# Kernel optimization log

Hardware: AMD Instinct MI355X
Metric: run time of the kernel (lower is better)

The kernel has to match this reference:

```python
import math
import jax, jax.numpy as jnp
import numpy as np

N_HEADS = 16
D_MODEL = 1024
B, S = 1, 2048


def setup_inputs() -> dict:
    key = jax.random.key(0)
    ks = jax.random.split(key, 8)
    stdv = 1.0 / math.sqrt(D_MODEL)
    def w(k):
        return jax.random.uniform(k, (D_MODEL, D_MODEL), jnp.float32, -stdv, stdv)
    return {
        "query": jax.random.normal(ks[0], (B, S, D_MODEL), jnp.float32),
        "key": jax.random.normal(ks[1], (B, S, D_MODEL), jnp.float32),
        "value": jax.random.normal(ks[2], (B, S, D_MODEL), jnp.float32),
        "attn_mask": jax.random.randint(ks[3], (B, S, S), 0, 2, jnp.int32),
        "W_q": w(ks[4]),
        "W_k": w(ks[5]),
        "W_v": w(ks[6]),
        "W_o": w(ks[7]),
    }


def reference(query, key, value, attn_mask, W_q, W_k, W_v, W_o):
    b = query.shape[0]
    d = D_MODEL // N_HEADS
    # F.linear(x, W) = x @ W.T
    def proj(x, W):
        y = jnp.einsum('bse,de->bsd', x, W)  # [B,S,D]
        return y.reshape(b, -1, N_HEADS, d).transpose(0, 2, 1, 3)  # [B,H,S,d]
    q = proj(query, W_q)
    k = proj(key, W_k)
    v = proj(value, W_v)
    scores = jnp.einsum('bhsd,bhtd->bhst', q, k) / math.sqrt(d)  # [B,H,S,S]
    # masked_fill with -1e-07 where mask is truthy (faithful to source)
    mask = (attn_mask != 0)[:, None, :, :]  # broadcast over heads
    scores = jnp.where(mask, jnp.float32(-1e-07), scores)
    attn_scores = jax.nn.softmax(scores, axis=-1)
    # Faithful quirk: output uses PRE-softmax scores, not attn_scores
    out = jnp.einsum('bhst,bhtd->bhsd', scores, v)
    concat = out.transpose(0, 2, 1, 3).reshape(b, -1, D_MODEL)
    output = jnp.einsum('bse,de->bsd', concat, W_o)
    return output, attn_scores
```

## Files before the change

kernel.cpp:

```cpp
#include <hip/hip_runtime.h>

#define S 2048
#define DM 1024
#define H 16
#define DH 64

typedef __attribute__((ext_vector_type(8))) short bf16x8;
typedef __attribute__((ext_vector_type(4))) float f32x4;
typedef __attribute__((ext_vector_type(4))) unsigned short u16x4;
typedef unsigned short u16;
typedef unsigned int u32;

__device__ __forceinline__ void split2(float x, u16& h, u16& l) {
  const u32 u = __float_as_uint(x);
  const u32 hu = u & 0xFFFF0000u;
  h = (u16)(hu >> 16);
  const float rem = x - __uint_as_float(hu);
  u32 r = __float_as_uint(rem);
  r += 0x7FFFu + ((r >> 16) & 1u);
  l = (u16)(r >> 16);
}

__device__ __forceinline__ void split2v(float x, u16x4& h4, u16x4& l4, int i) {
  u16 hh, ll;
  split2(x, hh, ll);
  h4[i] = hh; l4[i] = ll;
}

__device__ __forceinline__ f32x4 mfma3(bf16x8 ah, bf16x8 al, bf16x8 bh, bf16x8 bl, f32x4 c) {
  c = __builtin_amdgcn_mfma_f32_16x16x32_bf16(ah, bh, c, 0, 0, 0);
  c = __builtin_amdgcn_mfma_f32_16x16x32_bf16(ah, bl, c, 0, 0, 0);
  c = __builtin_amdgcn_mfma_f32_16x16x32_bf16(al, bh, c, 0, 0, 0);
  return c;
}

__global__ __launch_bounds__(256)
void qkv_proj(const float* __restrict__ q, const float* __restrict__ k,
              const float* __restrict__ v, const float* __restrict__ Wq,
              const float* __restrict__ Wk, const float* __restrict__ Wv,
              u16* __restrict__ qh, u16* __restrict__ ql,
              u16* __restrict__ kh, u16* __restrict__ kl,
              u16* __restrict__ vTh, u16* __restrict__ vTl)
{
  __shared__ u16 Ah[128][40], Al[128][40], Bh[128][40], Bl[128][40];
  const int tid = threadIdx.x;
  const int lane = tid & 63, w = tid >> 6;
  const int wr = w >> 1, wc = w & 1;
  const int lg = lane >> 4, lt = lane & 15;
  const int z = blockIdx.z;

  const float *A, *B;
  int m0, n0;
  if (z == 2) { A = Wv; B = v; m0 = blockIdx.y * 128; n0 = blockIdx.x * 128; }
  else {
    A = (z == 0) ? q : k; B = (z == 0) ? Wq : Wk;
    m0 = blockIdx.x * 128; n0 = blockIdx.y * 128;
  }

  f32x4 acc[4][4] = {};

  for (int k0 = 0; k0 < DM; k0 += 32) {
    float4 av[4], bv[4];
#pragma unroll
    for (int p = 0; p < 4; p++) {
      const int idx = p * 256 + tid;
      const int row = idx >> 3, c4 = (idx & 7) * 4;
      av[p] = *(const float4*)&A[(size_t)(m0 + row) * DM + k0 + c4];
      bv[p] = *(const float4*)&B[(size_t)(n0 + row) * DM + k0 + c4];
    }
    __syncthreads();
#pragma unroll
    for (int p = 0; p < 4; p++) {
      const int idx = p * 256 + tid;
      const int row = idx >> 3, c4 = (idx & 7) * 4;
      u16x4 h4, l4;
      split2v(av[p].x, h4, l4, 0); split2v(av[p].y, h4, l4, 1);
      split2v(av[p].z, h4, l4, 2); split2v(av[p].w, h4, l4, 3);
      *(u16x4*)&Ah[row][c4] = h4; *(u16x4*)&Al[row][c4] = l4;
      split2v(bv[p].x, h4, l4, 0); split2v(bv[p].y, h4, l4, 1);
      split2v(bv[p].z, h4, l4, 2); split2v(bv[p].w, h4, l4, 3);
      *(u16x4*)&Bh[row][c4] = h4; *(u16x4*)&Bl[row][c4] = l4;
    }
    __syncthreads();

    bf16x8 bhf[4], blf[4];
#pragma unroll
    for (int fj = 0; fj < 4; fj++) {
      const int r = wc * 64 + fj * 16 + lt;
      bhf[fj] = *(const bf16x8*)&Bh[r][lg * 8];
      blf[fj] = *(const bf16x8*)&Bl[r][lg * 8];
    }
#pragma unroll
    for (int fi = 0; fi < 4; fi++) {
      const int r = wr * 64 + fi * 16 + lt;
      const bf16x8 ahf = *(const bf16x8*)&Ah[r][lg * 8];
      const bf16x8 alf = *(const bf16x8*)&Al[r][lg * 8];
#pragma unroll
      for (int fj = 0; fj < 4; fj++)
        acc[fi][fj] = mfma3(ahf, alf, bhf[fj], blf[fj], acc[fi][fj]);
    }
  }

  u16 *dh, *dl;
  float scale;
  if (z == 0)      { dh = qh;  dl = ql;  scale = 0.125f; }
  else if (z == 1) { dh = kh;  dl = kl;  scale = 1.0f; }
  else             { dh = vTh; dl = vTl; scale = 1.0f; }

#pragma unroll
  for (int fi = 0; fi < 4; fi++)
#pragma unroll
    for (int r = 0; r < 4; r++) {
      const int m = m0 + wr * 64 + fi * 16 + lg * 4 + r;
#pragma unroll
      for (int fj = 0; fj < 4; fj++) {
        const int n = n0 + wc * 64 + fj * 16 + lt;
        const size_t addr = (z == 2) ? ((size_t)m * S + n)
                                     : ((size_t)((n >> 6) * S + m) * 64 + (n & 63));
        u16 hh, ll;
        split2(acc[fi][fj][r] * scale, hh, ll);
        dh[addr] = hh; dl[addr] = ll;
      }
    }
}

__global__ __launch_bounds__(256)
void attn_pv(const u16* __restrict__ qh, const u16* __restrict__ ql,
             const u16* __restrict__ kh, const u16* __restrict__ kl,
             const u16* __restrict__ vTh, const u16* __restrict__ vTl,
             const int* __restrict__ mask,
             float* __restrict__ attn, u16* __restrict__ ch, u16* __restrict__ cl)
{
  __shared__ u16 Kh[64][72], Kl[64][72];
  __shared__ u16 Vh[64][72], Vl[64][72];
  __shared__ u16 Ph[64][72], Pl[64][72];
  const int tid = threadIdx.x;
  const int lane = tid & 63, w = tid >> 6;
  const int lg = lane >> 4, lt = lane & 15;
  const int h = blockIdx.y, s0 = blockIdx.x * 64;
  const int qrow = s0 + w * 16 + lt;

  const size_t qbase = ((size_t)h * S + qrow) * 64;
  bf16x8 Qh_[2], Ql_[2];
  Qh_[0] = *(const bf16x8*)&qh[qbase + lg * 8];
  Qh_[1] = *(const bf16x8*)&qh[qbase + 32 + lg * 8];
  Ql_[0] = *(const bf16x8*)&ql[qbase + lg * 8];
  Ql_[1] = *(const bf16x8*)&ql[qbase + 32 + lg * 8];

  const size_t kbase = (size_t)h * S * 64;
  const size_t vbase = (size_t)h * 64 * S;

  f32x4 ao[4] = {};
  float m_run = -3.0e38f, l_run = 0.0f;

  for (int t0 = 0; t0 < S; t0 += 64) {
    __syncthreads();
#pragma unroll
    for (int p = 0; p < 2; p++) {
      const int chunk = p * 256 + tid;
      const int row = chunk >> 3, c8 = (chunk & 7) * 8;
      *(uint4*)&Kh[row][c8] = *(const uint4*)&kh[kbase + (size_t)(t0 + row) * 64 + c8];
      *(uint4*)&Kl[row][c8] = *(const uint4*)&kl[kbase + (size_t)(t0 + row) * 64 + c8];
      *(uint4*)&Vh[row][c8] = *(const uint4*)&vTh[vbase + (size_t)row * S + t0 + c8];
      *(uint4*)&Vl[row][c8] = *(const uint4*)&vTl[vbase + (size_t)row * S + t0 + c8];
    }
    __syncthreads();

    f32x4 sct[4] = {};
#pragma unroll
    for (int ks = 0; ks < 2; ks++) {
#pragma unroll
      for (int ft = 0; ft < 4; ft++) {
        const bf16x8 ah = *(const bf16x8*)&Kh[ft * 16 + lt][ks * 32 + lg * 8];
        const bf16x8 al = *(const bf16x8*)&Kl[ft * 16 + lt][ks * 32 + lg * 8];
        sct[ft] = mfma3(ah, al, Qh_[ks], Ql_[ks], sct[ft]);
      }
    }

    const int* mrow = &mask[(size_t)qrow * S + t0];
    float pm = -3.0e38f;
#pragma unroll
    for (int ft = 0; ft < 4; ft++) {
      const int tl = ft * 16 + lg * 4;
      const int4 mv = *(const int4*)&mrow[tl];
      f32x4 sv = sct[ft];
      sv[0] = mv.x ? -1e-7f : sv[0];
      sv[1] = mv.y ? -1e-7f : sv[1];
      sv[2] = mv.z ? -1e-7f : sv[2];
      sv[3] = mv.w ? -1e-7f : sv[3];
      sct[ft] = sv;
      pm = fmaxf(pm, fmaxf(fmaxf(sv[0], sv[1]), fmaxf(sv[2], sv[3])));
      u16x4 h4, l4;
      split2v(sv[0], h4, l4, 0); split2v(sv[1], h4, l4, 1);
      split2v(sv[2], h4, l4, 2); split2v(sv[3], h4, l4, 3);
      *(u16x4*)&Ph[w * 16 + lt][tl] = h4;
      *(u16x4*)&Pl[w * 16 + lt][tl] = l4;
    }

    pm = fmaxf(pm, __shfl_xor(pm, 16));
    pm = fmaxf(pm, __shfl_xor(pm, 32));
    const float mn = fmaxf(m_run, pm);
    float es = 0.0f;
#pragma unroll
    for (int ft = 0; ft < 4; ft++) {
      es += __expf(sct[ft][0] - mn) + __expf(sct[ft][1] - mn)
          + __expf(sct[ft][2] - mn) + __expf(sct[ft][3] - mn);
    }
    es += __shfl_xor(es, 16);
    es += __shfl_xor(es, 32);
    l_run = l_run * __expf(m_run - mn) + es;
    m_run = mn;

#pragma unroll
    for (int ks = 0; ks < 2; ks++) {
      const bf16x8 pa_h = *(const bf16x8*)&Ph[w * 16 + lt][ks * 32 + lg * 8];
      const bf16x8 pa_l = *(const bf16x8*)&Pl[w * 16 + lt][ks * 32 + lg * 8];
#pragma unroll
      for (int fd = 0; fd < 4; fd++) {
        const bf16x8 vb_h = *(const bf16x8*)&Vh[fd * 16 + lt][ks * 32 + lg * 8];
        const bf16x8 vb_l = *(const bf16x8*)&Vl[fd * 16 + lt][ks * 32 + lg * 8];
        ao[fd] = mfma3(pa_h, pa_l, vb_h, vb_l, ao[fd]);
      }
    }
  }

#pragma unroll
  for (int fd = 0; fd < 4; fd++)
#pragma unroll
    for (int r = 0; r < 4; r++) {
      const int qg = s0 + w * 16 + lg * 4 + r;
      const int d = h * 64 + fd * 16 + lt;
      u16 hh, ll;
      split2(ao[fd][r], hh, ll);
      ch[(size_t)qg * DM + d] = hh;
      cl[(size_t)qg * DM + d] = ll;
    }

  const float fm  = m_run;
  const float fil = 1.0f / l_run;

  for (int t0 = 0; t0 < S; t0 += 64) {
    __syncthreads();
#pragma unroll
    for (int p = 0; p < 2; p++) {
      const int chunk = p * 256 + tid;
      const int row = chunk >> 3, c8 = (chunk & 7) * 8;
      *(uint4*)&Kh[row][c8] = *(const uint4*)&kh[kbase + (size_t)(t0 + row) * 64 + c8];
      *(uint4*)&Kl[row][c8] = *(const uint4*)&kl[kbase + (size_t)(t0 + row) * 64 + c8];
    }
    __syncthreads();

    f32x4 sct[4] = {};
#pragma unroll
    for (int ks = 0; ks < 2; ks++) {
#pragma unroll
      for (int ft = 0; ft < 4; ft++) {
        const bf16x8 ah = *(const bf16x8*)&Kh[ft * 16 + lt][ks * 32 + lg * 8];
        const bf16x8 al = *(const bf16x8*)&Kl[ft * 16 + lt][ks * 32 + lg * 8];
        sct[ft] = mfma3(ah, al, Qh_[ks], Ql_[ks], sct[ft]);
      }
    }

    const int* mrow = &mask[(size_t)qrow * S + t0];
    float* arow = &attn[((size_t)h * S + qrow) * S + t0];
#pragma unroll
    for (int ft = 0; ft < 4; ft++) {
      const int tl = ft * 16 + lg * 4;
      const int4 mv = *(const int4*)&mrow[tl];
      f32x4 sv = sct[ft];
      sv[0] = mv.x ? -1e-7f : sv[0];
      sv[1] = mv.y ? -1e-7f : sv[1];
      sv[2] = mv.z ? -1e-7f : sv[2];
      sv[3] = mv.w ? -1e-7f : sv[3];
      const float4 o = make_float4(__expf(sv[0] - fm) * fil,
                                   __expf(sv[1] - fm) * fil,
                                   __expf(sv[2] - fm) * fil,
                                   __expf(sv[3] - fm) * fil);
      *(float4*)&arow[tl] = o;
    }
  }
}

__global__ __launch_bounds__(256)
void out_proj(const u16* __restrict__ ch, const u16* __restrict__ cl,
              const float* __restrict__ Wo, float* __restrict__ out)
{
  __shared__ u16 Ah[128][40], Al[128][40], Bh[128][40], Bl[128][40];
  const int tid = threadIdx.x;
  const int lane = tid & 63, w = tid >> 6;
  const int wr = w >> 1, wc = w & 1;
  const int lg = lane >> 4, lt = lane & 15;
  const int m0 = blockIdx.x * 128, n0 = blockIdx.y * 128;

  f32x4 acc[4][4] = {};

  for (int k0 = 0; k0 < DM; k0 += 32) {
    uint4 ahv[2], alv[2];
    float4 bv[4];
#pragma unroll
    for (int p = 0; p < 2; p++) {
      const int chunk = p * 256 + tid;
      const int row = chunk >> 2, c8 = (chunk & 3) * 8;
      ahv[p] = *(const uint4*)&ch[(size_t)(m0 + row) * DM + k0 + c8];
      alv[p] = *(const uint4*)&cl[(size_t)(m0 + row) * DM + k0 + c8];
    }
#pragma unroll
    for (int p = 0; p < 4; p++) {
      const int idx = p * 256 + tid;
      const int row = idx >> 3, c4 = (idx & 7) * 4;
      bv[p] = *(const float4*)&Wo[(size_t)(n0 + row) * DM + k0 + c4];
    }
    __syncthreads();
#pragma unroll
    for (int p = 0; p < 2; p++) {
      const int chunk = p * 256 + tid;
      const int row = chunk >> 2, c8 = (chunk & 3) * 8;
      *(uint4*)&Ah[row][c8] = ahv[p];
      *(uint4*)&Al[row][c8] = alv[p];
    }
#pragma unroll
    for (int p = 0; p < 4; p++) {
      const int idx = p * 256 + tid;
      const int row = idx >> 3, c4 = (idx & 7) * 4;
      u16x4 h4, l4;
      split2v(bv[p].x, h4, l4, 0); split2v(bv[p].y, h4, l4, 1);
      split2v(bv[p].z, h4, l4, 2); split2v(bv[p].w, h4, l4, 3);
      *(u16x4*)&Bh[row][c4] = h4; *(u16x4*)&Bl[row][c4] = l4;
    }
    __syncthreads();

    bf16x8 bhf[4], blf[4];
#pragma unroll
    for (int fj = 0; fj < 4; fj++) {
      const int r = wc * 64 + fj * 16 + lt;
      bhf[fj] = *(const bf16x8*)&Bh[r][lg * 8];
      blf[fj] = *(const bf16x8*)&Bl[r][lg * 8];
    }
#pragma unroll
    for (int fi = 0; fi < 4; fi++) {
      const int r = wr * 64 + fi * 16 + lt;
      const bf16x8 ahf = *(const bf16x8*)&Ah[r][lg * 8];
      const bf16x8 alf = *(const bf16x8*)&Al[r][lg * 8];
#pragma unroll
      for (int fj = 0; fj < 4; fj++)
        acc[fi][fj] = mfma3(ahf, alf, bhf[fj], blf[fj], acc[fi][fj]);
    }
  }

#pragma unroll
  for (int fi = 0; fi < 4; fi++)
#pragma unroll
    for (int r = 0; r < 4; r++) {
      const int m = m0 + wr * 64 + fi * 16 + lg * 4 + r;
#pragma unroll
      for (int fj = 0; fj < 4; fj++) {
        const int n = n0 + wc * 64 + fj * 16 + lt;
        out[(size_t)m * DM + n] = acc[fi][fj][r];
      }
    }
}

extern "C" void kernel_launch(void* const* d_in, const int* in_sizes, int n_in,
                              void* d_out, int out_size, void* d_ws, size_t ws_size,
                              hipStream_t stream)
{
  const float* query = (const float*)d_in[0];
  const float* key   = (const float*)d_in[1];
  const float* value = (const float*)d_in[2];
  const int*   mask  = (const int*)d_in[3];
  const float* Wq    = (const float*)d_in[4];
  const float* Wk    = (const float*)d_in[5];
  const float* Wv    = (const float*)d_in[6];
  const float* Wo    = (const float*)d_in[7];

  float* out  = (float*)d_out;
  float* attn = out + (size_t)S * DM;

  const size_t NE = (size_t)H * S * 64;
  u16* qh  = (u16*)d_ws;
  u16* ql  = qh  + NE;
  u16* kh  = ql  + NE;
  u16* kl  = kh  + NE;
  u16* vTh = kl  + NE;
  u16* vTl = vTh + NE;
  u16* ch  = vTl + NE;
  u16* cl  = ch  + NE;

  hipLaunchKernelGGL(qkv_proj, dim3(16, 8, 3), dim3(256), 0, stream,
                     query, key, value, Wq, Wk, Wv, qh, ql, kh, kl, vTh, vTl);

  hipLaunchKernelGGL(attn_pv, dim3(S / 64, H), dim3(256), 0, stream,
                     qh, ql, kh, kl, vTh, vTl, mask, attn, ch, cl);

  hipLaunchKernelGGL(out_proj, dim3(16, 8), dim3(256), 0, stream,
                     ch, cl, Wo, out);
}
```

Baseline: 579.6 us.

## Restructure attention kernel around 32x32 MFMA with register-resident P and split-key waves

```diff
diff --git a/kernel.cpp b/kernel.cpp
--- a/kernel.cpp
+++ b/kernel.cpp
@@ -7,7 +7,9 @@
 
 typedef __attribute__((ext_vector_type(8))) short bf16x8;
 typedef __attribute__((ext_vector_type(4))) float f32x4;
+typedef __attribute__((ext_vector_type(16))) float f32x16;
 typedef __attribute__((ext_vector_type(4))) unsigned short u16x4;
+typedef __attribute__((ext_vector_type(4))) unsigned int u32x4;
 typedef unsigned short u16;
 typedef unsigned int u32;
 
@@ -20,17 +22,32 @@
   r += 0x7FFFu + ((r >> 16) & 1u);
   l = (u16)(r >> 16);
 }
-
 __device__ __forceinline__ void split2v(float x, u16x4& h4, u16x4& l4, int i) {
   u16 hh, ll;
   split2(x, hh, ll);
   h4[i] = hh; l4[i] = ll;
 }
+__device__ __forceinline__ u32 pack_split_hi(float a, float b) {
+  return (__float_as_uint(a) >> 16) | (__float_as_uint(b) & 0xFFFF0000u);
+}
+__device__ __forceinline__ u32 pack_split_lo(float a, float b) {
+  const float ra = a - __uint_as_float(__float_as_uint(a) & 0xFFFF0000u);
+  const float rb = b - __uint_as_float(__float_as_uint(b) & 0xFFFF0000u);
+  u32 ua = __float_as_uint(ra); ua += 0x7FFFu + ((ua >> 16) & 1u);
+  u32 ub = __float_as_uint(rb); ub += 0x7FFFu + ((ub >> 16) & 1u);
+  return (ua >> 16) | (ub & 0xFFFF0000u);
+}
 
 __device__ __forceinline__ f32x4 mfma3(bf16x8 ah, bf16x8 al, bf16x8 bh, bf16x8 bl, f32x4 c) {
   c = __builtin_amdgcn_mfma_f32_16x16x32_bf16(ah, bh, c, 0, 0, 0);
   c = __builtin_amdgcn_mfma_f32_16x16x32_bf16(ah, bl, c, 0, 0, 0);
   c = __builtin_amdgcn_mfma_f32_16x16x32_bf16(al, bh, c, 0, 0, 0);
+  return c;
+}
+__device__ __forceinline__ f32x16 mfma3w(bf16x8 ah, bf16x8 al, bf16x8 bh, bf16x8 bl, f32x16 c) {
+  c = __builtin_amdgcn_mfma_f32_32x32x16_bf16(ah, bh, c, 0, 0, 0);
+  c = __builtin_amdgcn_mfma_f32_32x32x16_bf16(ah, bl, c, 0, 0, 0);
+  c = __builtin_amdgcn_mfma_f32_32x32x16_bf16(al, bh, c, 0, 0, 0);
   return c;
 }
 
@@ -124,33 +141,36 @@
     }
 }
 
-__global__ __launch_bounds__(256)
+__global__ __launch_bounds__(256, 3)
 void attn_pv(const u16* __restrict__ qh, const u16* __restrict__ ql,
              const u16* __restrict__ kh, const u16* __restrict__ kl,
              const u16* __restrict__ vTh, const u16* __restrict__ vTl,
              const int* __restrict__ mask,
              float* __restrict__ attn, u16* __restrict__ ch, u16* __restrict__ cl)
 {
-  __shared__ u16 Kh[64][72], Kl[64][72];
-  __shared__ u16 Vh[64][72], Vl[64][72];
-  __shared__ u16 Ph[64][72], Pl[64][72];
+  __shared__ u16 KV[4][64][72];
+  __shared__ float mbuf[2][64], lbuf[2][64];
+  float* sc = (float*)&KV[0][0][0];
+
   const int tid = threadIdx.x;
   const int lane = tid & 63, w = tid >> 6;
-  const int lg = lane >> 4, lt = lane & 15;
+  const int wq = w >> 1, wt = w & 1;
+  const int l31 = lane & 31, hi = lane >> 5;
   const int h = blockIdx.y, s0 = blockIdx.x * 64;
-  const int qrow = s0 + w * 16 + lt;
+  const int qrow = s0 + wq * 32 + l31;
 
   const size_t qbase = ((size_t)h * S + qrow) * 64;
-  bf16x8 Qh_[2], Ql_[2];
-  Qh_[0] = *(const bf16x8*)&qh[qbase + lg * 8];
-  Qh_[1] = *(const bf16x8*)&qh[qbase + 32 + lg * 8];
-  Ql_[0] = *(const bf16x8*)&ql[qbase + lg * 8];
-  Ql_[1] = *(const bf16x8*)&ql[qbase + 32 + lg * 8];
+  bf16x8 Qh_[4], Ql_[4];
+#pragma unroll
+  for (int ts = 0; ts < 4; ts++) {
+    Qh_[ts] = *(const bf16x8*)&qh[qbase + ts * 16 + hi * 8];
+    Ql_[ts] = *(const bf16x8*)&ql[qbase + ts * 16 + hi * 8];
+  }
 
   const size_t kbase = (size_t)h * S * 64;
   const size_t vbase = (size_t)h * 64 * S;
 
-  f32x4 ao[4] = {};
+  f32x16 ao0 = {}, ao1 = {};
   float m_run = -3.0e38f, l_run = 0.0f;
 
   for (int t0 = 0; t0 < S; t0 += 64) {
@@ -159,85 +179,117 @@
     for (int p = 0; p < 2; p++) {
       const int chunk = p * 256 + tid;
       const int row = chunk >> 3, c8 = (chunk & 7) * 8;
-      *(uint4*)&Kh[row][c8] = *(const uint4*)&kh[kbase + (size_t)(t0 + row) * 64 + c8];
-      *(uint4*)&Kl[row][c8] = *(const uint4*)&kl[kbase + (size_t)(t0 + row) * 64 + c8];
-      *(uint4*)&Vh[row][c8] = *(const uint4*)&vTh[vbase + (size_t)row * S + t0 + c8];
-      *(uint4*)&Vl[row][c8] = *(const uint4*)&vTl[vbase + (size_t)row * S + t0 + c8];
-    }
-    __syncthreads();
-
-    f32x4 sct[4] = {};
-#pragma unroll
-    for (int ks = 0; ks < 2; ks++) {
-#pragma unroll
-      for (int ft = 0; ft < 4; ft++) {
-        const bf16x8 ah = *(const bf16x8*)&Kh[ft * 16 + lt][ks * 32 + lg * 8];
-        const bf16x8 al = *(const bf16x8*)&Kl[ft * 16 + lt][ks * 32 + lg * 8];
-        sct[ft] = mfma3(ah, al, Qh_[ks], Ql_[ks], sct[ft]);
-      }
-    }
-
-    const int* mrow = &mask[(size_t)qrow * S + t0];
-    float pm = -3.0e38f;
-#pragma unroll
-    for (int ft = 0; ft < 4; ft++) {
-      const int tl = ft * 16 + lg * 4;
-      const int4 mv = *(const int4*)&mrow[tl];
-      f32x4 sv = sct[ft];
-      sv[0] = mv.x ? -1e-7f : sv[0];
-      sv[1] = mv.y ? -1e-7f : sv[1];
-      sv[2] = mv.z ? -1e-7f : sv[2];
-      sv[3] = mv.w ? -1e-7f : sv[3];
-      sct[ft] = sv;
-      pm = fmaxf(pm, fmaxf(fmaxf(sv[0], sv[1]), fmaxf(sv[2], sv[3])));
-      u16x4 h4, l4;
-      split2v(sv[0], h4, l4, 0); split2v(sv[1], h4, l4, 1);
-      split2v(sv[2], h4, l4, 2); split2v(sv[3], h4, l4, 3);
-      *(u16x4*)&Ph[w * 16 + lt][tl] = h4;
-      *(u16x4*)&Pl[w * 16 + lt][tl] = l4;
-    }
-
-    pm = fmaxf(pm, __shfl_xor(pm, 16));
+      *(uint4*)&KV[0][row][c8] = *(const uint4*)&kh[kbase + (size_t)(t0 + row) * 64 + c8];
+      *(uint4*)&KV[1][row][c8] = *(const uint4*)&kl[kbase + (size_t)(t0 + row) * 64 + c8];
+      *(uint4*)&KV[2][row][c8] = *(const uint4*)&vTh[vbase + (size_t)row * S + t0 + c8];
+      *(uint4*)&KV[3][row][c8] = *(const uint4*)&vTl[vbase + (size_t)row * S + t0 + c8];
+    }
+    __syncthreads();
+
+    const int* mrow = &mask[(size_t)qrow * S + t0 + wt * 32 + hi * 4];
+    const int4 mv0 = *(const int4*)&mrow[0];
+    const int4 mv1 = *(const int4*)&mrow[8];
+    const int4 mv2 = *(const int4*)&mrow[16];
+    const int4 mv3 = *(const int4*)&mrow[24];
+
+    f32x16 sct = {};
+#pragma unroll
+    for (int ts = 0; ts < 4; ts++) {
+      const bf16x8 ah = *(const bf16x8*)&KV[0][wt * 32 + l31][ts * 16 + hi * 8];
+      const bf16x8 al = *(const bf16x8*)&KV[1][wt * 32 + l31][ts * 16 + hi * 8];
+      sct = mfma3w(ah, al, Qh_[ts], Ql_[ts], sct);
+    }
+
+#define MSK(G, MV)                                              \
+    sct[4*G+0] = MV.x ? -1e-7f : sct[4*G+0];                    \
+    sct[4*G+1] = MV.y ? -1e-7f : sct[4*G+1];                    \
+    sct[4*G+2] = MV.z ? -1e-7f : sct[4*G+2];                    \
+    sct[4*G+3] = MV.w ? -1e-7f : sct[4*G+3];
+    MSK(0, mv0) MSK(1, mv1) MSK(2, mv2) MSK(3, mv3)
+
+    float pm = sct[0];
+#pragma unroll
+    for (int r = 1; r < 16; r++) pm = fmaxf(pm, sct[r]);
     pm = fmaxf(pm, __shfl_xor(pm, 32));
     const float mn = fmaxf(m_run, pm);
     float es = 0.0f;
 #pragma unroll
-    for (int ft = 0; ft < 4; ft++) {
-      es += __expf(sct[ft][0] - mn) + __expf(sct[ft][1] - mn)
-          + __expf(sct[ft][2] - mn) + __expf(sct[ft][3] - mn);
-    }
-    es += __shfl_xor(es, 16);
+    for (int r = 0; r < 16; r++) es += __expf(sct[r] - mn);
     es += __shfl_xor(es, 32);
     l_run = l_run * __expf(m_run - mn) + es;
     m_run = mn;
 
-#pragma unroll
-    for (int ks = 0; ks < 2; ks++) {
-      const bf16x8 pa_h = *(const bf16x8*)&Ph[w * 16 + lt][ks * 32 + lg * 8];
-      const bf16x8 pa_l = *(const bf16x8*)&Pl[w * 16 + lt][ks * 32 + lg * 8];
-#pragma unroll
-      for (int fd = 0; fd < 4; fd++) {
-        const bf16x8 vb_h = *(const bf16x8*)&Vh[fd * 16 + lt][ks * 32 + lg * 8];
-        const bf16x8 vb_l = *(const bf16x8*)&Vl[fd * 16 + lt][ks * 32 + lg * 8];
-        ao[fd] = mfma3(pa_h, pa_l, vb_h, vb_l, ao[fd]);
-      }
-    }
-  }
-
-#pragma unroll
-  for (int fd = 0; fd < 4; fd++)
-#pragma unroll
-    for (int r = 0; r < 4; r++) {
-      const int qg = s0 + w * 16 + lg * 4 + r;
-      const int d = h * 64 + fd * 16 + lt;
+    u32 ph0[4], ph1[4], pl0[4], pl1[4];
+#pragma unroll
+    for (int b = 0; b < 4; b++) {
+      ph0[b] = pack_split_hi(sct[4*b+0], sct[4*b+1]);
+      ph1[b] = pack_split_hi(sct[4*b+2], sct[4*b+3]);
+      pl0[b] = pack_split_lo(sct[4*b+0], sct[4*b+1]);
+      pl1[b] = pack_split_lo(sct[4*b+2], sct[4*b+3]);
+    }
+    u32 sph0[4], sph1[4], spl0[4], spl1[4];
+#pragma unroll
+    for (int b = 0; b < 4; b++) {
+      sph0[b] = (u32)__shfl_xor((int)ph0[b], 32);
+      sph1[b] = (u32)__shfl_xor((int)ph1[b], 32);
+      spl0[b] = (u32)__shfl_xor((int)pl0[b], 32);
+      spl1[b] = (u32)__shfl_xor((int)pl1[b], 32);
+    }
+
+#pragma unroll
+    for (int ts2 = 0; ts2 < 2; ts2++) {
+      const int b = 2 * ts2 + hi;
+      u32x4 wh, wl;
+      wh[0] = hi ? sph0[b] : ph0[b];  wh[1] = hi ? sph1[b] : ph1[b];
+      wh[2] = hi ? ph0[b] : sph0[b];  wh[3] = hi ? ph1[b] : sph1[b];
+      wl[0] = hi ? spl0[b] : pl0[b];  wl[1] = hi ? spl1[b] : pl1[b];
+      wl[2] = hi ? pl0[b] : spl0[b];  wl[3] = hi ? pl1[b] : spl1[b];
+      const bf16x8 pa_h = __builtin_bit_cast(bf16x8, wh);
+      const bf16x8 pa_l = __builtin_bit_cast(bf16x8, wl);
+
+      const int tc = wt * 32 + ts2 * 16 + hi * 8;
+      const bf16x8 vbh0 = *(const bf16x8*)&KV[2][l31][tc];
+      const bf16x8 vbl0 = *(const bf16x8*)&KV[3][l31][tc];
+      const bf16x8 vbh1 = *(const bf16x8*)&KV[2][32 + l31][tc];
+      const bf16x8 vbl1 = *(const bf16x8*)&KV[3][32 + l31][tc];
+      ao0 = mfma3w(pa_h, pa_l, vbh0, vbl0, ao0);
+      ao1 = mfma3w(pa_h, pa_l, vbh1, vbl1, ao1);
+    }
+  }
+
+  __syncthreads();
+  if (hi == 0) {
+    mbuf[wt][wq * 32 + l31] = m_run;
+    lbuf[wt][wq * 32 + l31] = l_run;
+  }
+  if (wt == 1) {
+#pragma unroll
+    for (int r = 0; r < 16; r++) {
+      const int qloc = wq * 32 + (r & 3) + 8 * (r >> 2) + 4 * hi;
+      sc[qloc * 64 + l31]      = ao0[r];
+      sc[qloc * 64 + 32 + l31] = ao1[r];
+    }
+  }
+  __syncthreads();
+  const float m0_ = mbuf[0][wq * 32 + l31], m1_ = mbuf[1][wq * 32 + l31];
+  const float l0_ = lbuf[0][wq * 32 + l31], l1_ = lbuf[1][wq * 32 + l31];
+  const float fm  = fmaxf(m0_, m1_);
+  const float fil = 1.0f / (l0_ * __expf(m0_ - fm) + l1_ * __expf(m1_ - fm));
+  if (wt == 0) {
+#pragma unroll
+    for (int r = 0; r < 16; r++) {
+      const int qloc = wq * 32 + (r & 3) + 8 * (r >> 2) + 4 * hi;
+      const float o0 = ao0[r] + sc[qloc * 64 + l31];
+      const float o1 = ao1[r] + sc[qloc * 64 + 32 + l31];
       u16 hh, ll;
-      split2(ao[fd][r], hh, ll);
-      ch[(size_t)qg * DM + d] = hh;
-      cl[(size_t)qg * DM + d] = ll;
-    }
-
-  const float fm  = m_run;
-  const float fil = 1.0f / l_run;
+      split2(o0, hh, ll);
+      ch[(size_t)(s0 + qloc) * DM + h * 64 + l31] = hh;
+      cl[(size_t)(s0 + qloc) * DM + h * 64 + l31] = ll;
+      split2(o1, hh, ll);
+      ch[(size_t)(s0 + qloc) * DM + h * 64 + 32 + l31] = hh;
+      cl[(size_t)(s0 + qloc) * DM + h * 64 + 32 + l31] = ll;
+    }
+  }
 
   for (int t0 = 0; t0 < S; t0 += 64) {
     __syncthreads();
@@ -245,38 +297,36 @@
     for (int p = 0; p < 2; p++) {
       const int chunk = p * 256 + tid;
       const int row = chunk >> 3, c8 = (chunk & 7) * 8;
-      *(uint4*)&Kh[row][c8] = *(const uint4*)&kh[kbase + (size_t)(t0 + row) * 64 + c8];
-      *(uint4*)&Kl[row][c8] = *(const uint4*)&kl[kbase + (size_t)(t0 + row) * 64 + c8];
-    }
-    __syncthreads();
-
-    f32x4 sct[4] = {};
-#pragma unroll
-    for (int ks = 0; ks < 2; ks++) {
-#pragma unroll
-      for (int ft = 0; ft < 4; ft++) {
-        const bf16x8 ah = *(const bf16x8*)&Kh[ft * 16 + lt][ks * 32 + lg * 8];
-        const bf16x8 al = *(const bf16x8*)&Kl[ft * 16 + lt][ks * 32 + lg * 8];
-        sct[ft] = mfma3(ah, al, Qh_[ks], Ql_[ks], sct[ft]);
-      }
-    }
-
-    const int* mrow = &mask[(size_t)qrow * S + t0];
-    float* arow = &attn[((size_t)h * S + qrow) * S + t0];
-#pragma unroll
-    for (int ft = 0; ft < 4; ft++) {
-      const int tl = ft * 16 + lg * 4;
-      const int4 mv = *(const int4*)&mrow[tl];
-      f32x4 sv = sct[ft];
-      sv[0] = mv.x ? -1e-7f : sv[0];
-      sv[1] = mv.y ? -1e-7f : sv[1];
-      sv[2] = mv.z ? -1e-7f : sv[2];
-      sv[3] = mv.w ? -1e-7f : sv[3];
-      const float4 o = make_float4(__expf(sv[0] - fm) * fil,
-                                   __expf(sv[1] - fm) * fil,
-                                   __expf(sv[2] - fm) * fil,
-                                   __expf(sv[3] - fm) * fil);
-      *(float4*)&arow[tl] = o;
+      *(uint4*)&KV[0][row][c8] = *(const uint4*)&kh[kbase + (size_t)(t0 + row) * 64 + c8];
+      *(uint4*)&KV[1][row][c8] = *(const uint4*)&kl[kbase + (size_t)(t0 + row) * 64 + c8];
+    }
+    __syncthreads();
+
+    const int* mrow = &mask[(size_t)qrow * S + t0 + wt * 32 + hi * 4];
+    const int4 mv0 = *(const int4*)&mrow[0];
+    const int4 mv1 = *(const int4*)&mrow[8];
+    const int4 mv2 = *(const int4*)&mrow[16];
+    const int4 mv3 = *(const int4*)&mrow[24];
+
+    f32x16 sct = {};
+#pragma unroll
+    for (int ts = 0; ts < 4; ts++) {
+      const bf16x8 ah = *(const bf16x8*)&KV[0][wt * 32 + l31][ts * 16 + hi * 8];
+      const bf16x8 al = *(const bf16x8*)&KV[1][wt * 32 + l31][ts * 16 + hi * 8];
+      sct = mfma3w(ah, al, Qh_[ts], Ql_[ts], sct);
+    }
+    MSK(0, mv0) MSK(1, mv1) MSK(2, mv2) MSK(3, mv3)
+#undef MSK
+
+    float* arow = &attn[((size_t)h * S + qrow) * S + t0 + wt * 32 + 4 * hi];
+#pragma unroll
+    for (int g = 0; g < 4; g++) {
+      float4 o;
+      o.x = __expf(sct[4*g+0] - fm) * fil;
+      o.y = __expf(sct[4*g+1] - fm) * fil;
+      o.z = __expf(sct[4*g+2] - fm) * fil;
+      o.w = __expf(sct[4*g+3] - fm) * fil;
+      *(float4*)&arow[8 * g] = o;
     }
   }
 }
```

New measurement: 703.9 us. 1.21x slower.
